# Kernel tuning notes

Hardware: AMD Instinct MI355X
Metric: run time of the kernel (lower is better)

Reference implementation:

```python
import jax, jax.numpy as jnp
import numpy as np

NBATCH, NELEC, NATOMS, NBAS, NORB = 1024, 64, 16, 256, 128

# per-atom shell pattern: (l, m) pairs; bas_n = l (standard for GTO primitives)
_SHELL_LM = [(0, 0), (1, -1), (1, 0), (1, 1), (2, -2), (2, -1), (2, 0), (2, 1), (2, 2),
             (0, 0), (1, -1), (1, 0), (1, 1), (2, 0), (2, 2), (2, -2)]


def _norm_gaussian(bas_exp, bas_n):
    # Torch _norm_gaussian: bas_n += 1; A = exp**(0.25*(2n+1)); B = 2**(2n+1.5);
    # C = factorial2(2n-1)*sqrt(pi); norm = sqrt(B/C)*A
    n1 = bas_n + 1.0
    A = bas_exp ** (0.25 * (2.0 * n1 + 1.0))
    B = 2.0 ** (2.0 * n1 + 1.5)
    # 2*n1-1 in {1,3,5} for n in {0,1,2}: factorial2 -> {1,3,15}
    f2 = np.array([1.0, 3.0, 15.0], dtype=np.float32)[bas_n.astype(np.int32)]
    C = f2 * np.float32(np.sqrt(np.pi))
    return (np.sqrt(B / C) * A).astype(np.float32)


def setup_inputs() -> dict:
    key = jax.random.key(0)
    k0, k1, k2, k3, k4 = jax.random.split(key, 5)
    inp = jax.random.normal(k0, (NBATCH, NELEC, 3), jnp.float32) * 2.0
    atom_coords = jax.random.normal(k1, (NATOMS, 3), jnp.float32) * 3.0
    bas_exp = jax.random.uniform(k2, (NBAS,), jnp.float32, minval=0.2, maxval=3.0)
    bas_coeffs = jax.random.uniform(k3, (NBAS,), jnp.float32, minval=0.5, maxval=1.0)

    lm = np.array(_SHELL_LM * (NBAS // len(_SHELL_LM)), dtype=np.int32)  # [NBAS,2]
    bas_l = jnp.asarray(lm[:, 0])
    bas_m = jnp.asarray(lm[:, 1])
    bas_n = jnp.asarray(lm[:, 0].astype(np.float32))
    bas_atom_index = jnp.asarray((np.arange(NBAS) // (NBAS // NATOMS)).astype(np.int32))
    index_ctr = jnp.sort(jax.random.randint(k4, (NBAS,), 0, NORB)).astype(jnp.int32)
    norm_cst = jnp.asarray(_norm_gaussian(np.asarray(bas_exp), np.asarray(bas_n)))
    return {
        'input': inp, 'atom_coords': atom_coords, 'bas_exp': bas_exp,
        'bas_coeffs': bas_coeffs, 'norm_cst': norm_cst, 'bas_n': bas_n,
        'bas_l': bas_l, 'bas_m': bas_m, 'bas_atom_index': bas_atom_index,
        'index_ctr': index_ctr,
    }


def _spherical_harmonics(xyz, r, r2, bas_l, bas_m):
    # real spherical harmonics up to l=2 (QMCTorch constants)
    x, y, z = xyz[..., 0], xyz[..., 1], xyz[..., 2]
    C0 = 0.2820948          # 1/(2 sqrt(pi))
    C1 = 0.4886025          # sqrt(3/(4 pi))
    C2XY = 1.0925484        # sqrt(15/(4 pi))
    C2Z2 = 0.31539156       # sqrt(5/(16 pi))
    C2D = 0.5462742         # sqrt(15/(16 pi))
    y1 = C1 * jnp.where(bas_m == -1, y, jnp.where(bas_m == 0, z, x)) / r
    y2 = jnp.where(bas_m == -2, C2XY * x * y,
         jnp.where(bas_m == -1, C2XY * y * z,
         jnp.where(bas_m == 0, C2Z2 * (2.0 * z * z - x * x - y * y),
         jnp.where(bas_m == 1, C2XY * z * x, C2D * (x * x - y * y))))) / r2
    return jnp.where(bas_l == 0, C0, jnp.where(bas_l == 1, y1, y2))


def reference(input, atom_coords, bas_exp, bas_coeffs, norm_cst, bas_n,
              bas_l, bas_m, bas_atom_index, index_ctr):
    # bas_coords = atom_coords.repeat_interleave(nshells) expressed as a gather
    bas_coords = atom_coords[bas_atom_index]                     # [nbas, 3]
    xyz = input[:, :, None, :] - bas_coords[None, None, :, :]    # [B, E, nbas, 3]
    r2 = jnp.sum(xyz * xyz, axis=-1)                             # [B, E, nbas]
    r = jnp.sqrt(r2)
    R = r ** bas_n * jnp.exp(-bas_exp * r2)                      # gaussian radial
    Y = _spherical_harmonics(xyz, r, r2, bas_l, bas_m)
    bas = norm_cst * bas_coeffs * R * Y                          # [B, E, nbas]
    ao = jnp.zeros((input.shape[0], input.shape[1], NORB), bas.dtype)
    return ao.at[:, :, index_ctr].add(bas)                       # index_add over dim 2
```

## Files before the change

### kernel.cpp

```cpp
#include <hip/hip_runtime.h>

#define NBAS  256
#define NORB  128
#define NROWS 65536
#define WPB   4
#define RPW   4
#define ROWS_PER_BLOCK (WPB * RPW)

__device__ __forceinline__ float wave_scan_incl(float x) {
    int t;
    t = __builtin_amdgcn_update_dpp(0, __float_as_int(x), 0x111, 0xf, 0xf, false);
    x += __int_as_float(t);
    t = __builtin_amdgcn_update_dpp(0, __float_as_int(x), 0x112, 0xf, 0xf, false);
    x += __int_as_float(t);
    t = __builtin_amdgcn_update_dpp(0, __float_as_int(x), 0x114, 0xf, 0xf, false);
    x += __int_as_float(t);
    t = __builtin_amdgcn_update_dpp(0, __float_as_int(x), 0x118, 0xf, 0xf, false);
    x += __int_as_float(t);
    t = __builtin_amdgcn_update_dpp(0, __float_as_int(x), 0x142, 0xa, 0xf, false);
    x += __int_as_float(t);
    t = __builtin_amdgcn_update_dpp(0, __float_as_int(x), 0x143, 0xc, 0xf, false);
    x += __int_as_float(t);
    return x;
}

__global__ __launch_bounds__(256, 6) void ao_kernel(
    const float* __restrict__ inp,
    const float* __restrict__ atom_coords,
    const float* __restrict__ bas_exp,
    const float* __restrict__ bas_coeffs,
    const float* __restrict__ norm_cst,
    const int*   __restrict__ bas_l,
    const int*   __restrict__ bas_m,
    const int*   __restrict__ bas_atom_index,
    const int*   __restrict__ index_ctr,
    float* __restrict__ out)
{
    __shared__ __align__(16) float s_buf[WPB][RPW][NBAS];
    __shared__ int s_start[NORB + 1];

    const int tid = threadIdx.x;
    const int w   = tid >> 6, ln = tid & 63;

    {
        int ic   = index_ctr[tid];
        int prev = (tid == 0) ? -1 : index_ctr[tid - 1];
        for (int o = prev + 1; o <= ic; ++o) s_start[o] = tid;
        if (tid == NBAS - 1)
            for (int o = ic + 1; o <= NORB; ++o) s_start[o] = NBAS;
    }

    const int l = bas_l[ln], m = bas_m[ln];
    float nex[4], lcc[4], cx[4], cy[4], cz[4];
    #pragma unroll
    for (int j = 0; j < 4; ++j) {
        int b = ln + 64 * j;
        nex[j] = -bas_exp[b] * 1.4426950408889634f;
        lcc[j] = __log2f(norm_cst[b] * bas_coeffs[b]);
        int ai = bas_atom_index[b];
        cx[j] = atom_coords[ai*3+0];
        cy[j] = atom_coords[ai*3+1];
        cz[j] = atom_coords[ai*3+2];
    }
    const float C0 = 0.2820948f, C1 = 0.4886025f, C2XY = 1.0925484f,
                C2Z2 = 0.31539156f, C2D = 0.5462742f;
    float a0=0.f,a1=0.f,a2=0.f,a3=0.f, b0=0.f,b1=0.f,b2=0.f,b3=0.f, c9=0.f;
    if (l == 0)            { a3 = C0; b3 = 1.f; }
    else if (l == 1) {
        b3 = 1.f;
        if      (m == -1) a1 = C1;
        else if (m ==  0) a2 = C1;
        else              a0 = C1;
    } else {
        if      (m == -2) { a0 = C2XY; b1 = 1.f; }
        else if (m == -1) { a1 = C2XY; b2 = 1.f; }
        else if (m ==  0) { a2 = 3.f*C2Z2; b2 = 1.f; c9 = -C2Z2; }
        else if (m ==  1) { a2 = C2XY; b0 = 1.f; }
        else              { a0 = C2D; a1 = C2D; b0 = 1.f; b1 = -1.f; }
    }

    __syncthreads();
    const int st0 = s_start[2*ln], st1 = s_start[2*ln+1], st2 = s_start[2*ln+2];

    const int rowbase = __builtin_amdgcn_readfirstlane(
        (int)blockIdx.x * ROWS_PER_BLOCK + w * RPW);
    float* bufw = &s_buf[w][0][0];

    #pragma unroll
    for (int r = 0; r < RPW; ++r) {
        const int row = rowbase + r;
        float px = inp[row*3+0], py = inp[row*3+1], pz = inp[row*3+2];
        float* buf = bufw + r * NBAS;
        #pragma unroll
        for (int j = 0; j < 4; ++j) {
            float x = px - cx[j], y = py - cy[j], z = pz - cz[j];
            float r2 = fmaf(x, x, fmaf(y, y, z * z));
            float A  = fmaf(a0, x, fmaf(a1, y, fmaf(a2, z, a3)));
            float Bv = fmaf(b0, x, fmaf(b1, y, fmaf(b2, z, b3)));
            float P  = fmaf(c9, r2, A * Bv);
            float E  = __builtin_exp2f(fmaf(nex[j], r2, lcc[j]));
            buf[ln + 64*j] = E * P;
        }
    }

    #pragma unroll
    for (int r = 0; r < RPW; ++r) {
        float* buf = bufw + r * NBAS;
        float4 v = *reinterpret_cast<const float4*>(&buf[ln << 2]);
        float e0 = v.x;
        float e1 = e0 + v.y;
        float e2 = e1 + v.z;
        float e3 = e2 + v.w;
        float s    = wave_scan_incl(e3);
        float excl = s - e3;
        *reinterpret_cast<float4*>(&buf[ln << 2]) =
            make_float4(e0 + excl, e1 + excl, e2 + excl, e3 + excl);
    }

    #pragma unroll
    for (int r = 0; r < RPW; ++r) {
        const float* buf = bufw + r * NBAS;
        float p0 = (st0 > 0) ? buf[st0 - 1] : 0.f;
        float p1 = (st1 > 0) ? buf[st1 - 1] : 0.f;
        float p2 = (st2 > 0) ? buf[st2 - 1] : 0.f;
        const int row = rowbase + r;
        *reinterpret_cast<float2*>(&out[(size_t)row * NORB + 2*ln]) =
            make_float2(p1 - p0, p2 - p1);
    }
}

extern "C" void kernel_launch(void* const* d_in, const int* in_sizes, int n_in,
                              void* d_out, int out_size, void* d_ws, size_t ws_size,
                              hipStream_t stream) {
    const float* inp   = (const float*)d_in[0];
    const float* atomc = (const float*)d_in[1];
    const float* bexp  = (const float*)d_in[2];
    const float* bcoef = (const float*)d_in[3];
    const float* bnorm = (const float*)d_in[4];
    const int* bl   = (const int*)d_in[6];
    const int* bm   = (const int*)d_in[7];
    const int* bai  = (const int*)d_in[8];
    const int* ictr = (const int*)d_in[9];
    float* out = (float*)d_out;

    hipLaunchKernelGGL(ao_kernel, dim3(NROWS / ROWS_PER_BLOCK), dim3(256), 0, stream,
                       inp, atomc, bexp, bcoef, bnorm, bl, bm, bai, ictr, out);
}
```

Measured before the change: 21.14 us.

## Precompute per-basis constants in a setup kernel and scan in registers

Moves the per-basis constant derivation (exponent scaling, log of norm times coefficient, atom coordinate gather, spherical-harmonic coefficients, orbital segment starts via binary search) into a tiny one-wave setup kernel that writes packed float4 records to workspace. The main kernel now only loads eight float4s per lane. It also performs the prefix scan directly on register values with DPP plus lane-63 broadcasts instead of a store/reload/scan through LDS. This trades a second kernel launch and a serialized dependency for less per-block prologue work and fewer LDS round-trips. Occupancy hint is lowered from 6 to 5.

```diff
diff --git a/kernel.cpp b/kernel.cpp
--- a/kernel.cpp
+++ b/kernel.cpp
@@ -24,8 +24,11 @@
     return x;
 }
 
-__global__ __launch_bounds__(256, 6) void ao_kernel(
-    const float* __restrict__ inp,
+__device__ __forceinline__ float bcast63(float x) {
+    return __int_as_float(__builtin_amdgcn_readlane(__float_as_int(x), 63));
+}
+
+__global__ void setup_kernel(
     const float* __restrict__ atom_coords,
     const float* __restrict__ bas_exp,
     const float* __restrict__ bas_coeffs,
@@ -34,22 +37,10 @@
     const int*   __restrict__ bas_m,
     const int*   __restrict__ bas_atom_index,
     const int*   __restrict__ index_ctr,
-    float* __restrict__ out)
+    float4* __restrict__ ws4)
 {
-    __shared__ __align__(16) float s_buf[WPB][RPW][NBAS];
-    __shared__ int s_start[NORB + 1];
-
-    const int tid = threadIdx.x;
-    const int w   = tid >> 6, ln = tid & 63;
-
-    {
-        int ic   = index_ctr[tid];
-        int prev = (tid == 0) ? -1 : index_ctr[tid - 1];
-        for (int o = prev + 1; o <= ic; ++o) s_start[o] = tid;
-        if (tid == NBAS - 1)
-            for (int o = ic + 1; o <= NORB; ++o) s_start[o] = NBAS;
-    }
-
+    const int ln = threadIdx.x;
+    if (ln >= 64) return;
     const int l = bas_l[ln], m = bas_m[ln];
     float nex[4], lcc[4], cx[4], cy[4], cz[4];
     #pragma unroll
@@ -78,19 +69,59 @@
         else if (m ==  1) { a2 = C2XY; b0 = 1.f; }
         else              { a0 = C2D; a1 = C2D; b0 = 1.f; b1 = -1.f; }
     }
+    int st[3];
+    #pragma unroll
+    for (int k = 0; k < 3; ++k) {
+        int o = 2*ln + k, lo = 0, hi = NBAS;
+        while (lo < hi) {
+            int mid = (lo + hi) >> 1;
+            if (index_ctr[mid] < o) lo = mid + 1; else hi = mid;
+        }
+        st[k] = lo;
+    }
+    ws4[0*64+ln] = make_float4(nex[0],nex[1],nex[2],nex[3]);
+    ws4[1*64+ln] = make_float4(lcc[0],lcc[1],lcc[2],lcc[3]);
+    ws4[2*64+ln] = make_float4(cx[0],cx[1],cx[2],cx[3]);
+    ws4[3*64+ln] = make_float4(cy[0],cy[1],cy[2],cy[3]);
+    ws4[4*64+ln] = make_float4(cz[0],cz[1],cz[2],cz[3]);
+    ws4[5*64+ln] = make_float4(a0,a1,a2,a3);
+    ws4[6*64+ln] = make_float4(b0,b1,b2,b3);
+    ws4[7*64+ln] = make_float4(c9, __int_as_float(st[0]),
+                               __int_as_float(st[1]), __int_as_float(st[2]));
+}
 
-    __syncthreads();
-    const int st0 = s_start[2*ln], st1 = s_start[2*ln+1], st2 = s_start[2*ln+2];
+__global__ __launch_bounds__(256, 5) void ao_kernel(
+    const float*  __restrict__ inp,
+    const float4* __restrict__ ws4,
+    float* __restrict__ out)
+{
+    __shared__ __align__(16) float s_pref[WPB][RPW][NBAS];
+
+    const int tid = threadIdx.x;
+    const int w   = tid >> 6, ln = tid & 63;
+
+    const float4 qn = ws4[0*64+ln], ql = ws4[1*64+ln];
+    const float4 qx = ws4[2*64+ln], qy = ws4[3*64+ln], qz = ws4[4*64+ln];
+    const float4 qa = ws4[5*64+ln], qb = ws4[6*64+ln], qc = ws4[7*64+ln];
+    const float nex[4] = {qn.x,qn.y,qn.z,qn.w};
+    const float lcc[4] = {ql.x,ql.y,ql.z,ql.w};
+    const float cx[4]  = {qx.x,qx.y,qx.z,qx.w};
+    const float cy[4]  = {qy.x,qy.y,qy.z,qy.w};
+    const float cz[4]  = {qz.x,qz.y,qz.z,qz.w};
+    const float a0=qa.x, a1=qa.y, a2=qa.z, a3=qa.w;
+    const float b0=qb.x, b1=qb.y, b2=qb.z, b3=qb.w;
+    const float c9=qc.x;
+    const int st0=__float_as_int(qc.y), st1=__float_as_int(qc.z), st2=__float_as_int(qc.w);
 
     const int rowbase = __builtin_amdgcn_readfirstlane(
         (int)blockIdx.x * ROWS_PER_BLOCK + w * RPW);
-    float* bufw = &s_buf[w][0][0];
+    float* bufw = &s_pref[w][0][0];
 
     #pragma unroll
     for (int r = 0; r < RPW; ++r) {
         const int row = rowbase + r;
         float px = inp[row*3+0], py = inp[row*3+1], pz = inp[row*3+2];
-        float* buf = bufw + r * NBAS;
+        float sc[4];
         #pragma unroll
         for (int j = 0; j < 4; ++j) {
             float x = px - cx[j], y = py - cy[j], z = pz - cz[j];
@@ -99,22 +130,17 @@
             float Bv = fmaf(b0, x, fmaf(b1, y, fmaf(b2, z, b3)));
             float P  = fmaf(c9, r2, A * Bv);
             float E  = __builtin_exp2f(fmaf(nex[j], r2, lcc[j]));
-            buf[ln + 64*j] = E * P;
+            sc[j] = wave_scan_incl(E * P);
         }
-    }
-
-    #pragma unroll
-    for (int r = 0; r < RPW; ++r) {
+        float t0 = bcast63(sc[0]);
+        float t1 = bcast63(sc[1]);
+        float t2 = bcast63(sc[2]);
+        float o1 = t0, o2 = t0 + t1, o3 = o2 + t2;
         float* buf = bufw + r * NBAS;
-        float4 v = *reinterpret_cast<const float4*>(&buf[ln << 2]);
-        float e0 = v.x;
-        float e1 = e0 + v.y;
-        float e2 = e1 + v.z;
-        float e3 = e2 + v.w;
-        float s    = wave_scan_incl(e3);
-        float excl = s - e3;
-        *reinterpret_cast<float4*>(&buf[ln << 2]) =
-            make_float4(e0 + excl, e1 + excl, e2 + excl, e3 + excl);
+        buf[ln      ] = sc[0];
+        buf[ln +  64] = sc[1] + o1;
+        buf[ln + 128] = sc[2] + o2;
+        buf[ln + 192] = sc[3] + o3;
     }
 
     #pragma unroll
@@ -141,8 +167,11 @@
     const int* bm   = (const int*)d_in[7];
     const int* bai  = (const int*)d_in[8];
     const int* ictr = (const int*)d_in[9];
-    float* out = (float*)d_out;
+    float*  out = (float*)d_out;
+    float4* ws4 = (float4*)d_ws;
 
+    hipLaunchKernelGGL(setup_kernel, dim3(1), dim3(64), 0, stream,
+                       atomc, bexp, bcoef, bnorm, bl, bm, bai, ictr, ws4);
     hipLaunchKernelGGL(ao_kernel, dim3(NROWS / ROWS_PER_BLOCK), dim3(256), 0, stream,
-                       inp, atomc, bexp, bcoef, bnorm, bl, bm, bai, ictr, out);
+                       inp, ws4, out);
 }
```

Result: slower. 29.15 us (+37.9%).
